# Optimization experiments

Measured on AMD Instinct MI355X. Metric: run time of the kernel, lower is better.

The kernel has to match this reference:

```python
import jax, jax.numpy as jnp
import numpy as np

PERIOD = 15          # hardcoded in the torch module's forward: STL(series, 15)
N_SEASONAL = 7       # statsmodels STL default seasonal smoother length
N_TREND = 29         # smallest odd >= 1.5*p/(1-1.5/7) = 28.64 -> 29 (statsmodels default)
N_LOWPASS = 17       # smallest odd > period (statsmodels default)
N_INNER = 2          # statsmodels: robust=False -> 2 inner iterations, 0 outer


def _loess_matrix(n, q, ts):
    """Dense linear operator for degree-1 LOESS smoothing of a length-n series
    evaluated at (possibly out-of-range) integer positions ts. Non-robust LOESS is
    linear in y, so smoothing == matmul with this constant matrix."""
    M = np.zeros((len(ts), n), dtype=np.float64)
    qq = min(q, n)
    for i, t in enumerate(ts):
        left = int(np.clip(t - (q - 1) // 2, 0, n - qq))
        right = left + qq - 1
        h = max(t - left, right - t)
        if q > n:
            h += (q - n) / 2.0
        xs = np.arange(left, right + 1, dtype=np.float64)
        w = np.clip(1.0 - (np.abs(xs - t) / h) ** 3, 0.0, None) ** 3  # tricube
        w = w / w.sum()
        xbar = (w * xs).sum()
        var = (w * (xs - xbar) ** 2).sum()
        a = w.copy()
        if var > 1e-12:  # degree-1 local linear fit; fall back to deg-0 if degenerate
            a = w * (1.0 + (t - xbar) * (xs - xbar) / var)
        M[i, left:right + 1] = a
    return M.astype(np.float32)


def _ma(x, k):
    """Moving average of window k along last axis (valid mode)."""
    cs = jnp.cumsum(x, axis=-1)
    cs = jnp.concatenate([jnp.zeros(x.shape[:-1] + (1,), x.dtype), cs], axis=-1)
    return (cs[..., k:] - cs[..., :-k]) / k


def setup_inputs() -> dict:
    key = jax.random.key(0)
    x = jax.random.normal(key, (128, 480, 256), dtype=jnp.float32)  # [B, T, C]
    return {"x": x}


def reference(x):
    B, T, Cc = x.shape
    p = PERIOD
    n_sub = T // p  # cycle-subseries length; T chosen divisible by period

    # Constant LOESS smoothing operators (numpy, baked in as jit constants)
    M_seas = jnp.asarray(_loess_matrix(n_sub, N_SEASONAL, np.arange(-1, n_sub + 1)))  # (n_sub+2, n_sub)
    M_lp = jnp.asarray(_loess_matrix(T, N_LOWPASS, np.arange(T)))                     # (T, T)
    M_trend = jnp.asarray(_loess_matrix(T, N_TREND, np.arange(T)))                    # (T, T)

    y = jnp.transpose(x, (0, 2, 1))  # [B, C, T]
    trend = jnp.zeros_like(y)
    seasonal = jnp.zeros_like(y)

    for _ in range(N_INNER):  # STL inner loop (Cleveland 1990, non-robust)
        # 1. detrend
        D = y - trend
        # 2. cycle-subseries LOESS smoothing, extended one period each side
        Dsub = D.reshape(B, Cc, n_sub, p)                      # subseries along axis 2
        Cext = jnp.einsum('sn,bcnp->bcsp', M_seas, Dsub)       # [B,C,n_sub+2,p]
        Cext = Cext.reshape(B, Cc, (n_sub + 2) * p)            # time order, length T+2p
        # 3. low-pass: MA(p) x2, MA(3), then LOESS(n_l)
        lp = _ma(_ma(_ma(Cext, p), p), 3)                      # length T
        L = jnp.einsum('tn,bcn->bct', M_lp, lp)
        # 4. seasonal = smoothed subseries (center T) minus low-pass
        seasonal = Cext[..., p:p + T] - L
        # 5+6. deseasonalize and trend LOESS
        trend = jnp.einsum('tn,bcn->bct', M_trend, y - seasonal)

    resid = y - seasonal - trend
    seas_plus_resid = jnp.transpose(seasonal + resid, (0, 2, 1))  # [B, T, C]
    trend_out = jnp.transpose(trend, (0, 2, 1))
    return (seas_plus_resid, trend_out)
```

## Files before the change

kernel.cpp:

```cpp
#include <hip/hip_runtime.h>
#include <hip/hip_bf16.h>
#include <stdint.h>

#define TLEN 480
#define NB 128
#define NC 256

typedef short bf16x8 __attribute__((ext_vector_type(8)));
typedef float f32x4 __attribute__((ext_vector_type(4)));
typedef unsigned short u16;
typedef unsigned int u32;

__device__ inline u16 f2bf(float f) {
    union { float f; uint32_t u; } v; v.f = f;
    uint32_t u = v.u;
    return (u16)((u + 0x7fffu + ((u >> 16) & 1u)) >> 16);
}

__device__ inline u32 pack2bf(float lo, float hi) {
    return __builtin_amdgcn_perm(__float_as_uint(hi), __float_as_uint(lo), 0x07060302u);
}

__device__ int loess_w(int t, int n, int q, float* out) {
    int left = t - (q - 1) / 2;
    if (left < 0) left = 0;
    if (left > n - q) left = n - q;
    int right = left + q - 1;
    int h = (t - left) > (right - t) ? (t - left) : (right - t);
    double w[29];
    double wsum = 0.0;
    for (int i = 0; i < q; ++i) {
        double dist = fabs((double)(left + i - t)) / (double)h;
        double u = 1.0 - dist * dist * dist;
        if (u < 0.0) u = 0.0;
        double wv = u * u * u;
        w[i] = wv; wsum += wv;
    }
    for (int i = 0; i < q; ++i) w[i] /= wsum;
    double xbar = 0.0;
    for (int i = 0; i < q; ++i) xbar += w[i] * (double)(left + i);
    double var = 0.0;
    for (int i = 0; i < q; ++i) { double d = (double)(left + i) - xbar; var += w[i] * d * d; }
    if (var > 1e-12) {
        double tb = (double)t - xbar;
        for (int i = 0; i < q; ++i) {
            double d = (double)(left + i) - xbar;
            out[i] = (float)(w[i] * (1.0 + tb * d / var));
        }
    } else {
        for (int i = 0; i < q; ++i) out[i] = (float)w[i];
    }
    return left;
}

__global__ void k_loess(float* Ms, float* w3, float* MlpC, float* MtC) {
    int gid = blockIdx.x * 256 + threadIdx.x;
    if (gid < 34) {
        float wl[7];
        int left = loess_w(gid - 1, 32, 7, wl);
        float* row = Ms + gid * 32;
        #pragma unroll
        for (int i = 0; i < 32; ++i) row[i] = 0.0f;
        for (int i = 0; i < 7; ++i) row[left + i] = wl[i];
    } else if (gid < 514) {
        int t = gid - 34;
        float wl[17];
        loess_w(t, TLEN, 17, wl);
        for (int i = 0; i < 17; ++i) MlpC[t * 17 + i] = wl[i];
    } else if (gid < 994) {
        int t = gid - 514;
        float wl[29];
        loess_w(t, TLEN, 29, wl);
        for (int i = 0; i < 29; ++i) MtC[t * 29 + i] = wl[i];
    } else if (gid == 994) {
        for (int d = 0; d <= 30; ++d) {
            int cnt = 0;
            for (int c = 0; c < 3; ++c)
                for (int a = 0; a < 15; ++a) {
                    int b = d - a - c;
                    if (b >= 0 && b < 15) cnt++;
                }
            w3[d] = (float)((double)cnt / 675.0);
        }
    }
}

__global__ void k_S(const float* __restrict__ Ms, const float* __restrict__ w3,
                    const float* __restrict__ MlpC, float* __restrict__ S) {
    int id = blockIdx.x * 256 + threadIdx.x;
    if (id >= TLEN * TLEN) return;
    int t = id / TLEN, u = id - t * TLEN;
    int nu = u / 15, ju = u - nu * 15;
    int slp = t - 8;
    if (slp < 0) slp = 0;
    if (slp > TLEN - 17) slp = TLEN - 17;
    float acc = 0.0f;
    for (int k = 0; k < 17; ++k) {
        int i = slp + k;
        int s_lo = (i - ju + 14) / 15;
        float g = 0.0f;
        #pragma unroll
        for (int ds = 0; ds < 3; ++ds) {
            int s = s_lo + ds;
            int d = s * 15 + ju - i;
            if (s >= 0 && s < 34 && d >= 0 && d <= 30)
                g += Ms[s * 32 + nu] * w3[d];
        }
        acc += MlpC[t * 17 + k] * g;
    }
    float val = -acc;
    if (t % 15 == ju) val += Ms[(1 + t / 15) * 32 + nu];
    S[id] = val;
}

__global__ void k_VU(const float* __restrict__ MtC, const float* __restrict__ S,
                     float* __restrict__ U, float* __restrict__ V) {
    int id = blockIdx.x * 256 + threadIdx.x;
    if (id >= TLEN * TLEN) return;
    int t = id / TLEN, u = id - t * TLEN;
    int st = t - 14;
    if (st < 0) st = 0;
    if (st > TLEN - 29) st = TLEN - 29;
    float acc = 0.0f;
    for (int k = 0; k < 29; ++k)
        acc += MtC[t * 29 + k] * S[(size_t)(st + k) * TLEN + u];
    float mt = (u >= st && u < st + 29) ? MtC[t * 29 + (u - st)] : 0.0f;
    V[id] = acc;
    U[id] = mt - acc;
}

__global__ void k_A(const float* __restrict__ U, const float* __restrict__ V,
                    u16* __restrict__ Abf) {
    __shared__ float Vs[16][17];
    __shared__ float Us[16][17];
    int tx = threadIdx.x, ty = threadIdx.y;
    int u = blockIdx.x * 16 + tx;
    int t = blockIdx.y * 16 + ty;
    float acc = 0.0f;
    for (int kt = 0; kt < 30; ++kt) {
        Vs[ty][tx] = V[(size_t)t * TLEN + kt * 16 + tx];
        Us[ty][tx] = U[(size_t)(kt * 16 + ty) * TLEN + u];
        __syncthreads();
        #pragma unroll
        for (int e = 0; e < 16; ++e) acc += Vs[ty][e] * Us[e][tx];
        __syncthreads();
    }
    Abf[(size_t)t * TLEN + u] = f2bf(U[(size_t)t * TLEN + u] + acc);
}

__global__ __launch_bounds__(256, 4)
void k_gemm(const u16* __restrict__ A, const float* __restrict__ x,
            float* __restrict__ out0, float* __restrict__ out1) {
    __shared__ u16 Xs[NC * 40];
    int b = blockIdx.x;
    int t0 = blockIdx.y * 48;
    int tid = threadIdx.x;
    int wave = tid >> 6, lane = tid & 63;
    int lane15 = lane & 15, quad = lane >> 4;
    int cw = wave * 64;

    const u16* bp[3];
    #pragma unroll
    for (int j = 0; j < 3; ++j)
        bp[j] = A + (size_t)(t0 + j * 16 + lane15) * TLEN + quad * 8;

    int kkq = tid >> 5;
    int wq  = tid & 31;
    int kq_sw = kkq ^ ((wq & 3) << 1);

    const float* xbase = x + (size_t)b * TLEN * NC;

    f32x4 acc[4][3] = {};
    for (int s = 0; s < 15; ++s) {
        int k0 = s * 32;
        if (s) __syncthreads();
        #pragma unroll
        for (int it = 0; it < 2; ++it) {
            int c0 = wq * 4 + it * 128;
            const float* xp = xbase + (size_t)(k0 + kkq * 4) * NC + c0;
            float4 r0 = *(const float4*)(xp);
            float4 r1 = *(const float4*)(xp + NC);
            float4 r2 = *(const float4*)(xp + 2 * NC);
            float4 r3 = *(const float4*)(xp + 3 * NC);
            u32* base32 = (u32*)Xs;
            int o0 = c0 * 20 + kq_sw * 2;
            uint2 w;
            w.x = pack2bf(r0.x, r1.x); w.y = pack2bf(r2.x, r3.x);
            *(uint2*)(base32 + o0) = w;
            w.x = pack2bf(r0.y, r1.y); w.y = pack2bf(r2.y, r3.y);
            *(uint2*)(base32 + o0 + 20) = w;
            w.x = pack2bf(r0.z, r1.z); w.y = pack2bf(r2.z, r3.z);
            *(uint2*)(base32 + o0 + 40) = w;
            w.x = pack2bf(r0.w, r1.w); w.y = pack2bf(r2.w, r3.w);
            *(uint2*)(base32 + o0 + 60) = w;
        }
        __syncthreads();

        bf16x8 af[4], bfr[3];
        #pragma unroll
        for (int i = 0; i < 4; ++i) {
            int c = cw + i * 16 + lane15;
            int qp = quad ^ ((c >> 2) & 3);
            af[i] = *(const bf16x8*)&Xs[c * 40 + qp * 8];
        }
        #pragma unroll
        for (int j = 0; j < 3; ++j) bfr[j] = *(const bf16x8*)(bp[j] + k0);
        #pragma unroll
        for (int i = 0; i < 4; ++i)
            #pragma unroll
            for (int j = 0; j < 3; ++j)
                acc[i][j] = __builtin_amdgcn_mfma_f32_16x16x32_bf16(af[i], bfr[j], acc[i][j], 0, 0, 0);
    }

    #pragma unroll
    for (int i = 0; i < 4; ++i) {
        #pragma unroll
        for (int j = 0; j < 3; ++j) {
            int t = t0 + j * 16 + lane15;
            int c = cw + i * 16 + quad * 4;
            size_t base = ((size_t)b * TLEN + t) * NC + c;
            f32x4 xv = *(const f32x4*)(x + base);
            f32x4 tv = acc[i][j];
            __builtin_nontemporal_store(tv, (f32x4*)(out1 + base));
            f32x4 sv = xv - tv;
            __builtin_nontemporal_store(sv, (f32x4*)(out0 + base));
        }
    }
}

extern "C" void kernel_launch(void* const* d_in, const int* in_sizes, int n_in,
                              void* d_out, int out_size, void* d_ws, size_t ws_size,
                              hipStream_t stream) {
    const float* x = (const float*)d_in[0];
    float* out0 = (float*)d_out;
    float* out1 = (float*)d_out + (size_t)NB * TLEN * NC;

    char* ws = (char*)d_ws;
    size_t oMs  = 0;
    size_t oW3  = oMs + 4352;
    size_t oLpC = oW3 + 128;
    size_t oMtC = oLpC + 32640;
    size_t oS   = oMtC + 55680;
    size_t oU   = oS + 921600;
    size_t oV   = oU + 921600;
    size_t oA   = oV + 921600;

    float* Ms   = (float*)(ws + oMs);
    float* w3   = (float*)(ws + oW3);
    float* MlpC = (float*)(ws + oLpC);
    float* MtC  = (float*)(ws + oMtC);
    float* S    = (float*)(ws + oS);
    float* U    = (float*)(ws + oU);
    float* V    = (float*)(ws + oV);
    u16*   Abf  = (u16*)(ws + oA);

    k_loess<<<4, 256, 0, stream>>>(Ms, w3, MlpC, MtC);
    k_S<<<900, 256, 0, stream>>>(Ms, w3, MlpC, S);
    k_VU<<<900, 256, 0, stream>>>(MtC, S, U, V);
    k_A<<<dim3(30, 30), dim3(16, 16), 0, stream>>>(U, V, Abf);
    k_gemm<<<dim3(NB, 10), 256, 0, stream>>>(Abf, x, out0, out1);
}
```

Baseline: 288.6 us.

## Double-buffer GEMM smem with register prefetch and retile to 96x128 blocks

After: 274.4 us. 1.05x faster.

```diff
diff --git a/kernel.cpp b/kernel.cpp
--- a/kernel.cpp
+++ b/kernel.cpp
@@ -72,16 +72,15 @@
         float wl[29];
         loess_w(t, TLEN, 29, wl);
         for (int i = 0; i < 29; ++i) MtC[t * 29 + i] = wl[i];
-    } else if (gid == 994) {
-        for (int d = 0; d <= 30; ++d) {
-            int cnt = 0;
-            for (int c = 0; c < 3; ++c)
-                for (int a = 0; a < 15; ++a) {
-                    int b = d - a - c;
-                    if (b >= 0 && b < 15) cnt++;
-                }
-            w3[d] = (float)((double)cnt / 675.0);
-        }
+    } else if (gid < 1025) {
+        int d = gid - 994;
+        int cnt = 0;
+        for (int c = 0; c < 3; ++c)
+            for (int a = 0; a < 15; ++a) {
+                int b = d - a - c;
+                if (b >= 0 && b < 15) cnt++;
+            }
+        w3[d] = (float)((double)cnt / 675.0);
     }
 }
 
@@ -151,80 +150,84 @@
 __global__ __launch_bounds__(256, 4)
 void k_gemm(const u16* __restrict__ A, const float* __restrict__ x,
             float* __restrict__ out0, float* __restrict__ out1) {
-    __shared__ u16 Xs[NC * 40];
+    __shared__ u16 Xs[2][128 * 40];
     int b = blockIdx.x;
-    int t0 = blockIdx.y * 48;
+    int t0 = blockIdx.y * 96;
+    int cz = blockIdx.z * 128;
     int tid = threadIdx.x;
     int wave = tid >> 6, lane = tid & 63;
     int lane15 = lane & 15, quad = lane >> 4;
-    int cw = wave * 64;
-
-    const u16* bp[3];
-    #pragma unroll
-    for (int j = 0; j < 3; ++j)
-        bp[j] = A + (size_t)(t0 + j * 16 + lane15) * TLEN + quad * 8;
+    int cw = wave * 32;
 
     int kkq = tid >> 5;
     int wq  = tid & 31;
     int kq_sw = kkq ^ ((wq & 3) << 1);
-
-    const float* xbase = x + (size_t)b * TLEN * NC;
-
-    f32x4 acc[4][3] = {};
+    int c0 = wq * 4;
+
+    const float* xp0 = x + (size_t)b * TLEN * NC + (size_t)(kkq * 4) * NC + cz + c0;
+
+    const u16* bp = A + (size_t)(t0 + lane15) * TLEN + quad * 8;
+
+    f32x4 acc[2][6] = {};
+
+    float4 r[4];
+    #pragma unroll
+    for (int q = 0; q < 4; ++q) r[q] = *(const float4*)(xp0 + q * NC);
+
+    #pragma unroll
     for (int s = 0; s < 15; ++s) {
-        int k0 = s * 32;
-        if (s) __syncthreads();
-        #pragma unroll
-        for (int it = 0; it < 2; ++it) {
-            int c0 = wq * 4 + it * 128;
-            const float* xp = xbase + (size_t)(k0 + kkq * 4) * NC + c0;
-            float4 r0 = *(const float4*)(xp);
-            float4 r1 = *(const float4*)(xp + NC);
-            float4 r2 = *(const float4*)(xp + 2 * NC);
-            float4 r3 = *(const float4*)(xp + 3 * NC);
-            u32* base32 = (u32*)Xs;
+        const int pb = s & 1;
+        const int k0 = s * 32;
+
+        {
+            u32* base32 = (u32*)Xs[pb];
             int o0 = c0 * 20 + kq_sw * 2;
             uint2 w;
-            w.x = pack2bf(r0.x, r1.x); w.y = pack2bf(r2.x, r3.x);
+            w.x = pack2bf(r[0].x, r[1].x); w.y = pack2bf(r[2].x, r[3].x);
             *(uint2*)(base32 + o0) = w;
-            w.x = pack2bf(r0.y, r1.y); w.y = pack2bf(r2.y, r3.y);
+            w.x = pack2bf(r[0].y, r[1].y); w.y = pack2bf(r[2].y, r[3].y);
             *(uint2*)(base32 + o0 + 20) = w;
-            w.x = pack2bf(r0.z, r1.z); w.y = pack2bf(r2.z, r3.z);
+            w.x = pack2bf(r[0].z, r[1].z); w.y = pack2bf(r[2].z, r[3].z);
             *(uint2*)(base32 + o0 + 40) = w;
-            w.x = pack2bf(r0.w, r1.w); w.y = pack2bf(r2.w, r3.w);
+            w.x = pack2bf(r[0].w, r[1].w); w.y = pack2bf(r[2].w, r[3].w);
             *(uint2*)(base32 + o0 + 60) = w;
         }
+
+        if (s < 14) {
+            const float* xp = xp0 + (size_t)(s + 1) * 32 * NC;
+            #pragma unroll
+            for (int q = 0; q < 4; ++q) r[q] = *(const float4*)(xp + q * NC);
+        }
+
         __syncthreads();
 
-        bf16x8 af[4], bfr[3];
-        #pragma unroll
-        for (int i = 0; i < 4; ++i) {
+        bf16x8 af[2];
+        #pragma unroll
+        for (int i = 0; i < 2; ++i) {
             int c = cw + i * 16 + lane15;
             int qp = quad ^ ((c >> 2) & 3);
-            af[i] = *(const bf16x8*)&Xs[c * 40 + qp * 8];
-        }
-        #pragma unroll
-        for (int j = 0; j < 3; ++j) bfr[j] = *(const bf16x8*)(bp[j] + k0);
-        #pragma unroll
-        for (int i = 0; i < 4; ++i)
-            #pragma unroll
-            for (int j = 0; j < 3; ++j)
-                acc[i][j] = __builtin_amdgcn_mfma_f32_16x16x32_bf16(af[i], bfr[j], acc[i][j], 0, 0, 0);
+            af[i] = *(const bf16x8*)&Xs[pb][c * 40 + qp * 8];
+        }
+        #pragma unroll
+        for (int j = 0; j < 6; ++j) {
+            bf16x8 bfr = *(const bf16x8*)(bp + (size_t)j * 16 * TLEN + k0);
+            acc[0][j] = __builtin_amdgcn_mfma_f32_16x16x32_bf16(af[0], bfr, acc[0][j], 0, 0, 0);
+            acc[1][j] = __builtin_amdgcn_mfma_f32_16x16x32_bf16(af[1], bfr, acc[1][j], 0, 0, 0);
+        }
     }
 
     #pragma unroll
-    for (int i = 0; i < 4; ++i) {
-        #pragma unroll
-        for (int j = 0; j < 3; ++j) {
-            int t = t0 + j * 16 + lane15;
-            int c = cw + i * 16 + quad * 4;
-            size_t base = ((size_t)b * TLEN + t) * NC + c;
-            f32x4 xv = *(const f32x4*)(x + base);
-            f32x4 tv = acc[i][j];
-            __builtin_nontemporal_store(tv, (f32x4*)(out1 + base));
-            f32x4 sv = xv - tv;
-            __builtin_nontemporal_store(sv, (f32x4*)(out0 + base));
-        }
+    for (int j = 0; j < 6; ++j) {
+        int t = t0 + j * 16 + lane15;
+        size_t rowb = ((size_t)b * TLEN + t) * NC + cz + cw + quad * 4;
+        f32x4 xv0 = *(const f32x4*)(x + rowb);
+        f32x4 xv1 = *(const f32x4*)(x + rowb + 16);
+        f32x4 tv0 = acc[0][j];
+        f32x4 tv1 = acc[1][j];
+        __builtin_nontemporal_store(tv0, (f32x4*)(out1 + rowb));
+        __builtin_nontemporal_store(tv1, (f32x4*)(out1 + rowb + 16));
+        __builtin_nontemporal_store(xv0 - tv0, (f32x4*)(out0 + rowb));
+        __builtin_nontemporal_store(xv1 - tv1, (f32x4*)(out0 + rowb + 16));
     }
 }
 
@@ -254,9 +257,9 @@
     float* V    = (float*)(ws + oV);
     u16*   Abf  = (u16*)(ws + oA);
 
-    k_loess<<<4, 256, 0, stream>>>(Ms, w3, MlpC, MtC);
+    k_loess<<<5, 256, 0, stream>>>(Ms, w3, MlpC, MtC);
     k_S<<<900, 256, 0, stream>>>(Ms, w3, MlpC, S);
     k_VU<<<900, 256, 0, stream>>>(MtC, S, U, V);
     k_A<<<dim3(30, 30), dim3(16, 16), 0, stream>>>(U, V, Abf);
-    k_gemm<<<dim3(NB, 10), 256, 0, stream>>>(Abf, x, out0, out1);
-}
+    k_gemm<<<dim3(NB, 5, 2), 256, 0, stream>>>(Abf, x, out0, out1);
+}
```
